# Kernel optimization log

Hardware: AMD Instinct MI355X
Metric: run time of the kernel (lower is better)

## Reference

```python
import jax, jax.numpy as jnp
import numpy as np

B, N, D = 1, 2048, 1024
L, H, DH = 4, 16, 64
INNER = H * DH            # 1024, == D
FF = int(D * 4.0)         # 4096 (GEGLU inner)
SCALE = DH ** -0.5
LN_EPS = 1e-5


def setup_inputs() -> dict:
    key = jax.random.key(0)
    ks = jax.random.split(key, 8)
    w = 0.02
    inp = {
        'x': jax.random.normal(ks[0], (B, N, D), jnp.float32),
        'mask': jnp.ones((B, N), dtype=bool),
        # stacked per-layer params (leading dim L)
        'Wqkv': jax.random.normal(ks[1], (L, D, 3 * INNER), jnp.float32) * w,
        'Wo': jax.random.normal(ks[2], (L, INNER, D), jnp.float32) * w,
        'bo': jnp.zeros((L, D), jnp.float32),
        'ln1_g': jnp.ones((L, D), jnp.float32),
        'ln1_b': jnp.zeros((L, D), jnp.float32),
        'ln2_g': jnp.ones((L, D), jnp.float32),
        'ln2_b': jnp.zeros((L, D), jnp.float32),
        'ls1': jnp.full((L, D), 0.1, jnp.float32),  # LayerScale init_eps=0.1 (depth<=18)
        'ls2': jnp.full((L, D), 0.1, jnp.float32),
        'W1': jax.random.normal(ks[3], (L, D, 2 * FF), jnp.float32) * w,
        'b1': jnp.zeros((L, 2 * FF), jnp.float32),
        'W2': jax.random.normal(ks[4], (L, FF, D), jnp.float32) * w,
        'b2': jnp.zeros((L, D), jnp.float32),
    }
    return inp


def _layernorm(x, g, b):
    mu = jnp.mean(x, axis=-1, keepdims=True)
    var = jnp.mean(jnp.square(x - mu), axis=-1, keepdims=True)
    return (x - mu) * jax.lax.rsqrt(var + LN_EPS) * g + b


def _forward(x, mask, Wqkv, Wo, bo, ln1_g, ln1_b, ln2_g, ln2_b, ls1, ls2, W1, b1, W2, b2):
    n = x.shape[1]
    causal = jnp.arange(n)[None, :] > jnp.arange(n)[:, None]  # True = masked
    valid = mask[:, None, None, :] & ~causal[None, None]       # (B,1,N,N) True = keep
    for l in range(L):
        # --- attention sublayer: x + LayerScale(PreNorm(Attn))(x) ---
        h = _layernorm(x, ln1_g[l], ln1_b[l])
        qkv = h @ Wqkv[l]                                      # (B,N,3*INNER)
        q, k, v = jnp.split(qkv, 3, axis=-1)
        q = q.reshape(B, n, H, DH).transpose(0, 2, 1, 3) * SCALE
        k = k.reshape(B, n, H, DH).transpose(0, 2, 1, 3)
        v = v.reshape(B, n, H, DH).transpose(0, 2, 1, 3)
        dots = jnp.einsum('bhid,bhjd->bhij', q, k)             # (B,H,N,N)
        neg = -jnp.finfo(dots.dtype).max
        dots = jnp.where(valid, dots, neg)
        attn = jax.nn.softmax(dots, axis=-1)                   # stable_softmax, temp=1
        o = jnp.einsum('bhij,bhjd->bhid', attn, v)
        o = o.transpose(0, 2, 1, 3).reshape(B, n, INNER)
        o = o @ Wo[l] + bo[l]
        x = x + o * ls1[l]
        # --- feedforward sublayer: x + LayerScale(PreNorm(GEGLU-FFN))(x) ---
        h = _layernorm(x, ln2_g[l], ln2_b[l])
        u = h @ W1[l] + b1[l]                                  # (B,N,2*FF)
        a, g = jnp.split(u, 2, axis=-1)
        f = (a * jax.nn.gelu(g, approximate=False)) @ W2[l] + b2[l]
        x = x + f * ls2[l]
    return x


def reference(x, mask, Wqkv, Wo, bo, ln1_g, ln1_b, ln2_g, ln2_b, ls1, ls2, W1, b1, W2, b2):
    return _forward(x, mask, Wqkv, Wo, bo, ln1_g, ln1_b, ln2_g, ln2_b, ls1, ls2, W1, b1, W2, b2)
```

## Files before the change

### kernel.cpp

```cpp
#include <hip/hip_runtime.h>
#include <hip/hip_bf16.h>
#include <math.h>

#define LN_EPS 1e-5f
#define ATT_SCALE 0.125f

typedef __bf16 bf16x8 __attribute__((ext_vector_type(8)));
typedef float f32x4 __attribute__((ext_vector_type(4)));

__device__ __forceinline__ unsigned short f2bf(float f){
  unsigned int u = __builtin_bit_cast(unsigned int, f);
  u += 0x7fffu + ((u >> 16) & 1u);
  return (unsigned short)(u >> 16);
}
__device__ __forceinline__ float bfbits2f(unsigned int lo16){
  return __builtin_bit_cast(float, lo16 << 16);
}

__global__ __launch_bounds__(256) void ln_kernel(
    const float* __restrict__ X, const float* __restrict__ g,
    const float* __restrict__ b, unsigned short* __restrict__ H)
{
  __shared__ float red[4];
  int row = blockIdx.x, t = threadIdx.x;
  const float4 xv = ((const float4*)(X + (size_t)row*1024))[t];
  float s = xv.x + xv.y + xv.z + xv.w;
  #pragma unroll
  for (int o=32;o;o>>=1) s += __shfl_down(s,o);
  if ((t&63)==0) red[t>>6] = s;
  __syncthreads();
  float mu = (red[0]+red[1]+red[2]+red[3]) * (1.f/1024.f);
  __syncthreads();
  float dx = xv.x-mu, dy = xv.y-mu, dz = xv.z-mu, dw = xv.w-mu;
  float s2 = dx*dx+dy*dy+dz*dz+dw*dw;
  #pragma unroll
  for (int o=32;o;o>>=1) s2 += __shfl_down(s2,o);
  if ((t&63)==0) red[t>>6] = s2;
  __syncthreads();
  float var = (red[0]+red[1]+red[2]+red[3]) * (1.f/1024.f);
  float rs = rsqrtf(var + LN_EPS);
  const float4 gv = ((const float4*)g)[t];
  const float4 bv = ((const float4*)b)[t];
  ushort4 o4;
  o4.x = f2bf(dx*rs*gv.x + bv.x);
  o4.y = f2bf(dy*rs*gv.y + bv.y);
  o4.z = f2bf(dz*rs*gv.z + bv.z);
  o4.w = f2bf(dw*rs*gv.w + bv.w);
  ((ushort4*)(H + (size_t)row*1024))[t] = o4;
}

template<int SK, int DO_LN>
__global__ __launch_bounds__(256) void redln_kernel(
    const unsigned short* __restrict__ P, float* __restrict__ X,
    const float* __restrict__ bias, const float* __restrict__ scale,
    const float* __restrict__ g, const float* __restrict__ b,
    unsigned short* __restrict__ H)
{
  __shared__ float red[4];
  int row = blockIdx.x, t = threadIdx.x;
  size_t off = (size_t)row*1024 + t*4;
  float4 xv = *(const float4*)(X + off);
  float4 pv;
  {
    uint2 u = *(const uint2*)(P + off);
    pv.x = bfbits2f(u.x & 0xffffu); pv.y = bfbits2f(u.x >> 16);
    pv.z = bfbits2f(u.y & 0xffffu); pv.w = bfbits2f(u.y >> 16);
  }
  #pragma unroll
  for (int c=1;c<SK;c++){
    uint2 u = *(const uint2*)(P + (size_t)c*2048*1024 + off);
    pv.x += bfbits2f(u.x & 0xffffu); pv.y += bfbits2f(u.x >> 16);
    pv.z += bfbits2f(u.y & 0xffffu); pv.w += bfbits2f(u.y >> 16);
  }
  const float4 bv = ((const float4*)bias)[t];
  const float4 sv = ((const float4*)scale)[t];
  xv.x += (pv.x+bv.x)*sv.x;
  xv.y += (pv.y+bv.y)*sv.y;
  xv.z += (pv.z+bv.z)*sv.z;
  xv.w += (pv.w+bv.w)*sv.w;
  *(float4*)(X + off) = xv;
  if (DO_LN){
    float s = xv.x + xv.y + xv.z + xv.w;
    #pragma unroll
    for (int o=32;o;o>>=1) s += __shfl_down(s,o);
    if ((t&63)==0) red[t>>6] = s;
    __syncthreads();
    float mu = (red[0]+red[1]+red[2]+red[3]) * (1.f/1024.f);
    __syncthreads();
    float dx = xv.x-mu, dy = xv.y-mu, dz = xv.z-mu, dw = xv.w-mu;
    float s2 = dx*dx+dy*dy+dz*dz+dw*dw;
    #pragma unroll
    for (int o=32;o;o>>=1) s2 += __shfl_down(s2,o);
    if ((t&63)==0) red[t>>6] = s2;
    __syncthreads();
    float var = (red[0]+red[1]+red[2]+red[3]) * (1.f/1024.f);
    float rs = rsqrtf(var + LN_EPS);
    const float4 gv = ((const float4*)g)[t];
    const float4 lbv = ((const float4*)b)[t];
    ushort4 o4;
    o4.x = f2bf(dx*rs*gv.x + lbv.x);
    o4.y = f2bf(dy*rs*gv.y + lbv.y);
    o4.z = f2bf(dz*rs*gv.z + lbv.z);
    o4.w = f2bf(dw*rs*gv.w + lbv.w);
    ((ushort4*)(H + (size_t)row*1024))[t] = o4;
  }
}

__global__ __launch_bounds__(256) void trc_kernel(
    const float* __restrict__ W, unsigned short* __restrict__ WT, int K, int N)
{
  __shared__ float tile[64][65];
  int n0 = blockIdx.x*64, k0 = blockIdx.y*64;
  int t = threadIdx.x;
  int tx = t & 63, ty = t >> 6;
  #pragma unroll
  for (int p=0;p<16;p++){
    int r = ty*16+p;
    tile[r][tx] = W[(size_t)(k0+r)*N + n0 + tx];
  }
  __syncthreads();
  int kc = t & 31, tb = t >> 5;
  #pragma unroll
  for (int p=0;p<8;p++){
    int nr = tb + p*8;
    unsigned int lo = f2bf(tile[2*kc][nr]);
    unsigned int hi = f2bf(tile[2*kc+1][nr]);
    ((unsigned int*)(WT + (size_t)(n0+nr)*K + k0))[kc] = lo | (hi<<16);
  }
}

__global__ __launch_bounds__(256) void trc_w1_kernel(
    const float* __restrict__ W, unsigned short* __restrict__ WT)
{
  __shared__ float tile[64][65];
  int n0 = blockIdx.x*64, k0 = blockIdx.y*64;
  int ca = (n0>>5)*16;
  int t = threadIdx.x;
  int tx = t & 63, ty = t >> 6;
  #pragma unroll
  for (int p=0;p<16;p++){
    int r = ty*16+p;
    int col = (tx < 32) ? (ca + tx) : (ca + 4064 + tx);
    tile[r][tx] = W[(size_t)(k0+r)*8192 + col];
  }
  __syncthreads();
  int kc = t & 31, tb = t >> 5;
  #pragma unroll
  for (int p=0;p<8;p++){
    int nr = tb + p*8;
    int rr = nr & 31;
    int vcol = (nr>>5)*16 + (rr&15) + ((rr>>4)<<5);
    unsigned int lo = f2bf(tile[2*kc][vcol]);
    unsigned int hi = f2bf(tile[2*kc+1][vcol]);
    ((unsigned int*)(WT + (size_t)(n0+nr)*1024 + k0))[kc] = lo | (hi<<16);
  }
}

template<int MODE, int SWZ>
__global__ __launch_bounds__(256) void gemm_bt(
    const unsigned short* __restrict__ A, const unsigned short* __restrict__ BT,
    int M, int N, int K,
    unsigned short* __restrict__ Obf,
    const float* __restrict__ bias)
{
  __shared__ unsigned short Asm[2][128*64];
  __shared__ unsigned short Bsm[2][128*64];
  int t = threadIdx.x;
  int lane = t & 63;
  int w = t >> 6, wm = w >> 1, wn = w & 1;

  int bn, bm;
  if (SWZ){
    int nwg = gridDim.x * gridDim.y;
    int wg = blockIdx.y * gridDim.x + blockIdx.x;
    int cpx = nwg >> 3;
    int swz = (wg & 7) * cpx + (wg >> 3);
    bn = swz % gridDim.x; bm = swz / gridDim.x;
  } else {
    bn = blockIdx.x; bm = blockIdx.y;
  }

  f32x4 acc[4][4] = {};
  int ktBeg = 0, ktEnd = K >> 6;
  if (MODE == 3){
    int per = (K >> 6) / gridDim.z;
    ktBeg = blockIdx.z * per;
    ktEnd = ktBeg + per;
  }

  int srow = t >> 3, ssc = t & 7;
  auto STAGE = [&](int kt, int buf){
    #pragma unroll
    for (int c=0;c<4;c++){
      int row = c*32 + srow;
      int gc = ssc ^ (row & 7);
      const unsigned short* sa = A  + (size_t)(bm*128 + row)*K + kt*64 + gc*8;
      const unsigned short* sb = BT + (size_t)(bn*128 + row)*K + kt*64 + gc*8;
      __builtin_amdgcn_global_load_lds(
        (const __attribute__((address_space(1))) unsigned int*)sa,
        (__attribute__((address_space(3))) unsigned int*)(&Asm[buf][(c*256 + (t & ~63))*8]),
        16, 0, 0);
      __builtin_amdgcn_global_load_lds(
        (const __attribute__((address_space(1))) unsigned int*)sb,
        (__attribute__((address_space(3))) unsigned int*)(&Bsm[buf][(c*256 + (t & ~63))*8]),
        16, 0, 0);
    }
  };

  STAGE(ktBeg, 0);
  __syncthreads();
  int cur = 0;
  for (int kt = ktBeg; kt < ktEnd; ++kt){
    if (kt + 1 < ktEnd) STAGE(kt + 1, cur ^ 1);
    #pragma unroll
    for (int kk=0;kk<2;kk++){
      bf16x8 aF[4], bF[4];
      #pragma unroll
      for (int m=0;m<4;m++){
        int row = wm*64 + m*16 + (lane&15);
        int ch = kk*4 + (lane>>4);
        aF[m] = *(const bf16x8*)&Asm[cur][row*64 + (ch ^ (row&7))*8];
      }
      #pragma unroll
      for (int n=0;n<4;n++){
        int row = wn*64 + n*16 + (lane&15);
        int ch = kk*4 + (lane>>4);
        bF[n] = *(const bf16x8*)&Bsm[cur][row*64 + (ch ^ (row&7))*8];
      }
      __builtin_amdgcn_s_setprio(1);
      #pragma unroll
      for (int m=0;m<4;m++)
        #pragma unroll
        for (int n=0;n<4;n++)
          acc[m][n] = __builtin_amdgcn_mfma_f32_16x16x32_bf16(aF[m], bF[n], acc[m][n], 0,0,0);
      __builtin_amdgcn_s_setprio(0);
    }
    __syncthreads();
    cur ^= 1;
  }

  int colg = lane & 15;
  if (MODE==4){
    float b1a[2], b1g[2];
    #pragma unroll
    for (int p=0;p<2;p++){
      int oc = (bn*4 + wn*2 + p)*16 + colg;
      b1a[p] = bias[oc];
      b1g[p] = bias[oc + 4096];
    }
    #pragma unroll
    for (int m=0;m<4;m++){
      int gr0 = bm*128 + wm*64 + m*16 + (lane>>4)*4;
      #pragma unroll
      for (int p=0;p<2;p++){
        int ocol = (bn*4 + wn*2 + p)*16 + colg;
        #pragma unroll
        for (int j=0;j<4;j++){
          float va = acc[m][2*p][j]   + b1a[p];
          float vg = acc[m][2*p+1][j] + b1g[p];
          float f = va * (0.5f * vg * (1.f + erff(vg * 0.70710678118f)));
          Obf[(size_t)(gr0+j)*4096 + ocol] = f2bf(f);
        }
      }
    }
    return;
  }
  #pragma unroll
  for (int m=0;m<4;m++){
    int gr0 = bm*128 + wm*64 + m*16 + (lane>>4)*4;
    #pragma unroll
    for (int n=0;n<4;n++){
      int gc = bn*128 + wn*64 + n*16 + colg;
      #pragma unroll
      for (int j=0;j<4;j++){
        int gr = gr0 + j;
        float v = acc[m][n][j];
        if (MODE==0){
          Obf[(size_t)gr*N + gc] = f2bf(v);
        } else {
          Obf[(size_t)blockIdx.z*((size_t)M*N) + (size_t)gr*N + gc] = f2bf(v);
        }
      }
    }
  }
}

__global__ __launch_bounds__(256) void vtr_kernel(
    const unsigned short* __restrict__ qkv, unsigned short* __restrict__ VT)
{
  __shared__ unsigned int tile[64][33];
  int h = blockIdx.y;
  int n0 = blockIdx.x * 64;
  int t = threadIdx.x;
  #pragma unroll
  for (int p=0;p<8;p++){
    int idx = p*256 + t;
    int r = idx >> 5, c = idx & 31;
    tile[r][c] = *(const unsigned int*)(qkv + (size_t)(n0+r)*3072 + 2048 + h*64 + c*2);
  }
  __syncthreads();
  #pragma unroll
  for (int p=0;p<8;p++){
    int idx = p*256 + t;
    int d = idx >> 5, c = idx & 31;
    unsigned int a = tile[2*c][d>>1];
    unsigned int b = tile[2*c+1][d>>1];
    unsigned int lo = (d&1) ? (a>>16) : (a & 0xffffu);
    unsigned int hi = (d&1) ? (b>>16) : (b & 0xffffu);
    *(unsigned int*)(VT + (size_t)h*131072 + (size_t)d*2048 + n0 + c*2) = lo | (hi<<16);
  }
}

__global__ __launch_bounds__(256) void flash_attn(
    const unsigned short* __restrict__ qkv,
    const unsigned short* __restrict__ VT,
    unsigned short* __restrict__ O)
{
  __shared__ unsigned short Klds[2][64*64];
  __shared__ unsigned short Vlds[2][64*64];
  __shared__ unsigned short Plds[4][16*72];
  __shared__ float fbuf[4][16];
  __shared__ float lbuf[4][16];

  int t = threadIdx.x;
  int lane = t & 63;
  int w = t >> 6;
  int q15 = lane & 15, l16 = lane >> 4;

  int bid = blockIdx.x;
  int x = bid & 7, r = bid >> 3;
  int h = 2*x + (r & 1);
  int q = r >> 1;
  int qt = (q < 16) ? q : 47 - q;
  int q0 = qt * 64;

  bf16x8 qF[2];
  int qrow = q0 + w*16 + q15;
  #pragma unroll
  for (int db=0; db<2; db++)
    qF[db] = *(const bf16x8*)(qkv + (size_t)qrow*3072 + h*64 + db*32 + l16*8);

  int srow = t >> 3, ssc = t & 7;
  auto STAGE = [&](int kt, int buf){
    int k0 = kt*64;
    #pragma unroll
    for (int c=0;c<2;c++){
      int row = c*32 + srow;
      int gc = ssc ^ (row & 7);
      const unsigned short* sk = qkv + (size_t)(k0+row)*3072 + 1024 + h*64 + gc*8;
      const unsigned short* sv = VT + (size_t)h*131072 + (size_t)row*2048 + k0 + gc*8;
      __builtin_amdgcn_global_load_lds(
        (const __attribute__((address_space(1))) unsigned int*)sk,
        (__attribute__((address_space(3))) unsigned int*)(&Klds[buf][(c*256 + (t & ~63))*8]),
        16, 0, 0);
      __builtin_amdgcn_global_load_lds(
        (const __attribute__((address_space(1))) unsigned int*)sv,
        (__attribute__((address_space(3))) unsigned int*)(&Vlds[buf][(c*256 + (t & ~63))*8]),
        16, 0, 0);
    }
  };

  f32x4 o[4] = {};
  float m_run = -1e30f, l_run = 0.f;

  STAGE(0, 0);
  __syncthreads();
  int cur = 0;
  for (int kt = 0; kt <= qt; ++kt){
    if (kt < qt) STAGE(kt + 1, cur ^ 1);

    f32x4 s[4] = {};
    #pragma unroll
    for (int km=0;km<4;km++){
      #pragma unroll
      for (int db=0;db<2;db++){
        int row = km*16 + q15;
        int ch = db*4 + l16;
        bf16x8 kF = *(const bf16x8*)&Klds[cur][row*64 + (ch ^ (row&7))*8];
        s[km] = __builtin_amdgcn_mfma_f32_16x16x32_bf16(kF, qF[db], s[km], 0,0,0);
      }
    }

    bool diag = (kt == qt);
    float pmax = -1e30f;
    #pragma unroll
    for (int km=0;km<4;km++){
      #pragma unroll
      for (int j=0;j<4;j++){
        float sv = s[km][j] * ATT_SCALE;
        if (diag){
          int kg = km*16 + l16*4 + j;
          int qg = w*16 + q15;
          if (kg > qg) sv = -1e30f;
        }
        s[km][j] = sv;
        pmax = fmaxf(pmax, sv);
      }
    }
    pmax = fmaxf(pmax, __shfl_xor(pmax, 16));
    pmax = fmaxf(pmax, __shfl_xor(pmax, 32));

    float m_new = fmaxf(m_run, pmax);
    float f = __expf(m_run - m_new);

    float lsum = 0.f;
    #pragma unroll
    for (int km=0;km<4;km++){
      float p0 = __expf(s[km][0]-m_new);
      float p1 = __expf(s[km][1]-m_new);
      float p2 = __expf(s[km][2]-m_new);
      float p3 = __expf(s[km][3]-m_new);
      lsum += (p0+p1)+(p2+p3);
      unsigned int u0 = (unsigned int)f2bf(p0) | ((unsigned int)f2bf(p1)<<16);
      unsigned int u1 = (unsigned int)f2bf(p2) | ((unsigned int)f2bf(p3)<<16);
      *(uint2*)&Plds[w][q15*72 + km*16 + l16*4] = make_uint2(u0,u1);
    }
    lsum += __shfl_xor(lsum,16);
    lsum += __shfl_xor(lsum,32);
    l_run = l_run * f + lsum;
    m_run = m_new;

    if (l16 == 0) fbuf[w][q15] = f;
    f32x4 fv = *(f32x4*)&fbuf[w][l16*4];
    #pragma unroll
    for (int n=0;n<4;n++) o[n] *= fv;

    #pragma unroll
    for (int kb=0;kb<2;kb++){
      bf16x8 aP = *(const bf16x8*)&Plds[w][q15*72 + kb*32 + l16*8];
      #pragma unroll
      for (int n=0;n<4;n++){
        int row = n*16 + q15;
        int ch = kb*4 + l16;
        bf16x8 vF = *(const bf16x8*)&Vlds[cur][row*64 + (ch ^ (row&7))*8];
        o[n] = __builtin_amdgcn_mfma_f32_16x16x32_bf16(aP, vF, o[n], 0,0,0);
      }
    }
    __syncthreads();
    cur ^= 1;
  }

  if (l16 == 0) lbuf[w][q15] = 1.f / l_run;
  f32x4 lv = *(f32x4*)&lbuf[w][l16*4];

  #pragma unroll
  for (int n=0;n<4;n++){
    #pragma unroll
    for (int j=0;j<4;j++){
      int row = q0 + w*16 + l16*4 + j;
      int col = h*64 + n*16 + q15;
      O[(size_t)row*1024 + col] = f2bf(o[n][j]*lv[j]);
    }
  }
}

extern "C" void kernel_launch(void* const* d_in, const int* in_sizes, int n_in,
                              void* d_out, int out_size, void* d_ws, size_t ws_size,
                              hipStream_t stream)
{
  (void)in_sizes; (void)n_in; (void)out_size; (void)ws_size;
  const float* x_in = (const float*)d_in[0];
  const float* Wqkv = (const float*)d_in[2];
  const float* Wo   = (const float*)d_in[3];
  const float* bo   = (const float*)d_in[4];
  const float* ln1g = (const float*)d_in[5];
  const float* ln1b = (const float*)d_in[6];
  const float* ln2g = (const float*)d_in[7];
  const float* ln2b = (const float*)d_in[8];
  const float* ls1  = (const float*)d_in[9];
  const float* ls2  = (const float*)d_in[10];
  const float* W1   = (const float*)d_in[11];
  const float* b1   = (const float*)d_in[12];
  const float* W2   = (const float*)d_in[13];
  const float* b2   = (const float*)d_in[14];
  float* X = (float*)d_out;

  char* ws = (char*)d_ws;
  unsigned short* WT  = (unsigned short*)(ws);
  unsigned short* hb  = (unsigned short*)(ws + (16u<<20));
  unsigned short* qu  = (unsigned short*)(ws + (20u<<20));
  unsigned short* VTg = (unsigned short*)(ws + (36u<<20));
  unsigned short* of  = (unsigned short*)(ws + (52u<<20));
  unsigned short* PTb = (unsigned short*)(ws + (20u<<20));

  hipMemcpyAsync(d_out, (const void*)x_in, (size_t)2048*1024*4,
                 hipMemcpyDeviceToDevice, stream);

  for (int l = 0; l < 4; ++l){
    if (l == 0)
      ln_kernel<<<2048,256,0,stream>>>(X, ln1g, ln1b, hb);
    trc_kernel<<<dim3(3072/64,1024/64),256,0,stream>>>(Wqkv + (size_t)l*1024*3072, WT, 1024, 3072);
    gemm_bt<0,0><<<dim3(3072/128,2048/128),256,0,stream>>>(hb, WT, 2048,3072,1024,
        qu, nullptr);
    vtr_kernel<<<dim3(32,16),256,0,stream>>>(qu, VTg);
    flash_attn<<<512,256,0,stream>>>(qu, VTg, of);
    trc_kernel<<<dim3(1024/64,1024/64),256,0,stream>>>(Wo + (size_t)l*1024*1024, WT, 1024, 1024);
    gemm_bt<3,1><<<dim3(1024/128,2048/128,2),256,0,stream>>>(of, WT, 2048,1024,1024,
        PTb, nullptr);
    redln_kernel<2,1><<<2048,256,0,stream>>>(PTb, X, bo + l*1024, ls1 + l*1024,
        ln2g + l*1024, ln2b + l*1024, hb);
    trc_w1_kernel<<<dim3(8192/64,1024/64),256,0,stream>>>(W1 + (size_t)l*1024*8192, WT);
    gemm_bt<4,0><<<dim3(8192/128,2048/128),256,0,stream>>>(hb, WT, 2048,8192,1024,
        of, b1 + (size_t)l*8192);
    trc_kernel<<<dim3(1024/64,4096/64),256,0,stream>>>(W2 + (size_t)l*4096*1024, WT, 4096, 1024);
    gemm_bt<3,1><<<dim3(1024/128,2048/128,4),256,0,stream>>>(of, WT, 2048,1024,4096,
        PTb, nullptr);
    if (l < 3)
      redln_kernel<4,1><<<2048,256,0,stream>>>(PTb, X, b2 + l*1024, ls2 + l*1024,
          ln1g + (l+1)*1024, ln1b + (l+1)*1024, hb);
    else
      redln_kernel<4,0><<<2048,256,0,stream>>>(PTb, X, b2 + l*1024, ls2 + l*1024,
          nullptr, nullptr, nullptr);
  }
}
```

Baseline: 789.6 us.

## Add 256x256 8-wave pipelined GEMM for FFN W1/W2 projections

Adds a new 512-thread GEMM kernel with 256x256 output tiles that stages tiles straight into LDS with global_load_lds and interleaves half-tile loads with MFMA quarters behind explicit vmcnt waits and barriers. It replaces the 128x128 kernel for the GEGLU W1 GEMM (fused epilogue moved over) and for the W2 split-K GEMM. The W2 split-K factor goes from 4 to 8, so the reduce kernel now sums 8 partials. The aim is more data reuse per block and better load/compute overlap on the largest GEMMs, at the cost of heavier LDS and register use and a larger partial-sum buffer and reduction.

Measured after the change: 802.2 us. No clear change (+1.6%).

```diff
diff --git a/kernel.cpp b/kernel.cpp
--- a/kernel.cpp
+++ b/kernel.cpp
@@ -240,31 +240,6 @@
   }
 
   int colg = lane & 15;
-  if (MODE==4){
-    float b1a[2], b1g[2];
-    #pragma unroll
-    for (int p=0;p<2;p++){
-      int oc = (bn*4 + wn*2 + p)*16 + colg;
-      b1a[p] = bias[oc];
-      b1g[p] = bias[oc + 4096];
-    }
-    #pragma unroll
-    for (int m=0;m<4;m++){
-      int gr0 = bm*128 + wm*64 + m*16 + (lane>>4)*4;
-      #pragma unroll
-      for (int p=0;p<2;p++){
-        int ocol = (bn*4 + wn*2 + p)*16 + colg;
-        #pragma unroll
-        for (int j=0;j<4;j++){
-          float va = acc[m][2*p][j]   + b1a[p];
-          float vg = acc[m][2*p+1][j] + b1g[p];
-          float f = va * (0.5f * vg * (1.f + erff(vg * 0.70710678118f)));
-          Obf[(size_t)(gr0+j)*4096 + ocol] = f2bf(f);
-        }
-      }
-    }
-    return;
-  }
   #pragma unroll
   for (int m=0;m<4;m++){
     int gr0 = bm*128 + wm*64 + m*16 + (lane>>4)*4;
@@ -280,6 +255,166 @@
         } else {
           Obf[(size_t)blockIdx.z*((size_t)M*N) + (size_t)gr*N + gc] = f2bf(v);
         }
+      }
+    }
+  }
+}
+
+#define G8_BARRIER() do { asm volatile("" ::: "memory"); \
+  __builtin_amdgcn_s_barrier(); asm volatile("" ::: "memory"); \
+  __builtin_amdgcn_sched_barrier(0); } while(0)
+#define G8_VW6() asm volatile("s_waitcnt vmcnt(6)" ::: "memory")
+
+template<int MODE>
+__global__ __launch_bounds__(512,2) void gemm8p(
+    const unsigned short* __restrict__ A, const unsigned short* __restrict__ BT,
+    int M, int N, int K,
+    unsigned short* __restrict__ Obf, const float* __restrict__ bias)
+{
+  __shared__ __attribute__((aligned(16))) unsigned short lds[65536];
+  int t = threadIdx.x;
+  int lane = t & 63;
+  int w = t >> 6;
+  int wm = w >> 2, wn = w & 3;
+  int q15 = lane & 15, l16 = lane >> 4;
+
+  int bn = blockIdx.x, bm = blockIdx.y;
+  int rA0 = bm*256, rB0 = bn*256;
+
+  int nkt = K >> 6, ktBeg = 0;
+  if (MODE == 3){
+    int per = nkt / gridDim.z;
+    ktBeg = blockIdx.z * per;
+    nkt = per;
+  }
+
+  int u0 = (w*2+0)*8 + (lane>>3);
+  int u1 = (w*2+1)*8 + (lane>>3);
+  int c0 = (lane&7) ^ (u0&7);
+  int c1 = (lane&7) ^ (u1&7);
+
+  auto STAGE_A = [&](int ktg, int h, int buf){
+    int r0 = (u0&63) | (h<<6) | ((u0>>6)<<7);
+    int r1 = (u1&63) | (h<<6) | ((u1>>6)<<7);
+    const unsigned short* s0 = A + (size_t)(rA0 + r0)*K + ktg*64 + c0*8;
+    const unsigned short* s1 = A + (size_t)(rA0 + r1)*K + ktg*64 + c1*8;
+    __builtin_amdgcn_global_load_lds(
+      (const __attribute__((address_space(1))) unsigned int*)s0,
+      (__attribute__((address_space(3))) unsigned int*)(&lds[buf*32768 + h*8192 + (w*2+0)*512]),
+      16, 0, 0);
+    __builtin_amdgcn_global_load_lds(
+      (const __attribute__((address_space(1))) unsigned int*)s1,
+      (__attribute__((address_space(3))) unsigned int*)(&lds[buf*32768 + h*8192 + (w*2+1)*512]),
+      16, 0, 0);
+  };
+  auto STAGE_B = [&](int ktg, int h, int buf){
+    int r0 = (u0&31) | (h<<5) | ((u0>>5)<<6);
+    int r1 = (u1&31) | (h<<5) | ((u1>>5)<<6);
+    const unsigned short* s0 = BT + (size_t)(rB0 + r0)*K + ktg*64 + c0*8;
+    const unsigned short* s1 = BT + (size_t)(rB0 + r1)*K + ktg*64 + c1*8;
+    __builtin_amdgcn_global_load_lds(
+      (const __attribute__((address_space(1))) unsigned int*)s0,
+      (__attribute__((address_space(3))) unsigned int*)(&lds[buf*32768 + 16384 + h*8192 + (w*2+0)*512]),
+      16, 0, 0);
+    __builtin_amdgcn_global_load_lds(
+      (const __attribute__((address_space(1))) unsigned int*)s1,
+      (__attribute__((address_space(3))) unsigned int*)(&lds[buf*32768 + 16384 + h*8192 + (w*2+1)*512]),
+      16, 0, 0);
+  };
+
+  f32x4 acc[8][4] = {};
+  bf16x8 aF[4][2], bF0[2][2], bF1[2][2];
+
+#define G8_LOAD_AF(H, BASE) \
+  _Pragma("unroll") for (int m=0;m<4;m++){ \
+    int u = m*16 + q15 + wm*64; \
+    _Pragma("unroll") for (int kk=0;kk<2;kk++) \
+      aF[m][kk] = *(const bf16x8*)&lds[(BASE) + (H)*8192 + u*64 + (((kk*4+l16) ^ (u&7))*8)]; }
+#define G8_LOAD_BF(DST, H, BASE) \
+  _Pragma("unroll") for (int nn=0;nn<2;nn++){ \
+    int u = nn*16 + q15 + wn*32; \
+    _Pragma("unroll") for (int kk=0;kk<2;kk++) \
+      DST[nn][kk] = *(const bf16x8*)&lds[(BASE) + 16384 + (H)*8192 + u*64 + (((kk*4+l16) ^ (u&7))*8)]; }
+#define G8_QMFMA(MB, NB, BF) \
+  __builtin_amdgcn_s_setprio(1); \
+  _Pragma("unroll") for (int m=0;m<4;m++) \
+  _Pragma("unroll") for (int nn=0;nn<2;nn++) \
+  _Pragma("unroll") for (int kk=0;kk<2;kk++) \
+    acc[(MB)+m][(NB)+nn] = __builtin_amdgcn_mfma_f32_16x16x32_bf16( \
+        aF[m][kk], BF[nn][kk], acc[(MB)+m][(NB)+nn], 0,0,0); \
+  __builtin_amdgcn_s_setprio(0);
+
+  STAGE_A(ktBeg+0, 0, 0);
+  STAGE_A(ktBeg+0, 1, 0);
+  STAGE_B(ktBeg+0, 0, 0);
+  STAGE_B(ktBeg+0, 1, 0);
+  if (nkt > 1) STAGE_B(ktBeg+1, 0, 1);
+  asm volatile("s_waitcnt vmcnt(2)" ::: "memory");
+  G8_BARRIER();
+
+  for (int kt = 0; kt < nkt; ++kt){
+    int buf = kt & 1, obuf = buf ^ 1;
+    int base = buf * 32768;
+    if (kt + 1 < nkt) STAGE_A(ktBeg+kt+1, 0, obuf);
+    G8_VW6();
+    G8_BARRIER();
+    G8_LOAD_AF(0, base);
+    G8_LOAD_BF(bF0, 0, base);
+    G8_QMFMA(0, 0, bF0);
+    G8_BARRIER();
+    if (kt + 1 < nkt) STAGE_A(ktBeg+kt+1, 1, obuf);
+    G8_VW6();
+    G8_BARRIER();
+    G8_LOAD_BF(bF1, 1, base);
+    G8_QMFMA(0, 2, bF1);
+    G8_BARRIER();
+    if (kt + 1 < nkt) STAGE_B(ktBeg+kt+1, 1, obuf);
+    G8_VW6();
+    G8_BARRIER();
+    G8_LOAD_AF(1, base);
+    G8_QMFMA(4, 0, bF0);
+    G8_BARRIER();
+    if (kt + 2 < nkt) STAGE_B(ktBeg+kt+2, 0, buf);
+    G8_VW6();
+    G8_BARRIER();
+    G8_QMFMA(4, 2, bF1);
+    G8_BARRIER();
+  }
+
+  if (MODE == 4){
+    float b1a[2], b1g[2];
+    #pragma unroll
+    for (int p=0;p<2;p++){
+      int oc = (bn*8 + wn*2 + p)*16 + q15;
+      b1a[p] = bias[oc];
+      b1g[p] = bias[oc + 4096];
+    }
+    #pragma unroll
+    for (int m=0;m<8;m++){
+      int gr0 = bm*256 + wm*128 + m*16 + l16*4;
+      #pragma unroll
+      for (int p=0;p<2;p++){
+        int ocol = (bn*8 + wn*2 + p)*16 + q15;
+        #pragma unroll
+        for (int j=0;j<4;j++){
+          float va = acc[m][2*p][j]   + b1a[p];
+          float vg = acc[m][2*p+1][j] + b1g[p];
+          float f = va * (0.5f * vg * (1.f + erff(vg * 0.70710678118f)));
+          Obf[(size_t)(gr0+j)*4096 + ocol] = f2bf(f);
+        }
+      }
+    }
+  } else {
+    size_t zoff = (size_t)blockIdx.z * ((size_t)M*N);
+    #pragma unroll
+    for (int m=0;m<8;m++){
+      int gr0 = bm*256 + wm*128 + m*16 + l16*4;
+      #pragma unroll
+      for (int n=0;n<4;n++){
+        int gc = bn*256 + wn*64 + n*16 + q15;
+        #pragma unroll
+        for (int j=0;j<4;j++)
+          Obf[zoff + (size_t)(gr0+j)*N + gc] = f2bf(acc[m][n][j]);
       }
     }
   }
@@ -411,9 +546,9 @@
       float p2 = __expf(s[km][2]-m_new);
       float p3 = __expf(s[km][3]-m_new);
       lsum += (p0+p1)+(p2+p3);
-      unsigned int u0 = (unsigned int)f2bf(p0) | ((unsigned int)f2bf(p1)<<16);
-      unsigned int u1 = (unsigned int)f2bf(p2) | ((unsigned int)f2bf(p3)<<16);
-      *(uint2*)&Plds[w][q15*72 + km*16 + l16*4] = make_uint2(u0,u1);
+      unsigned int v0 = (unsigned int)f2bf(p0) | ((unsigned int)f2bf(p1)<<16);
+      unsigned int v1 = (unsigned int)f2bf(p2) | ((unsigned int)f2bf(p3)<<16);
+      *(uint2*)&Plds[w][q15*72 + km*16 + l16*4] = make_uint2(v0,v1);
     }
     lsum += __shfl_xor(lsum,16);
     lsum += __shfl_xor(lsum,32);
@@ -500,16 +635,16 @@
     redln_kernel<2,1><<<2048,256,0,stream>>>(PTb, X, bo + l*1024, ls1 + l*1024,
         ln2g + l*1024, ln2b + l*1024, hb);
     trc_w1_kernel<<<dim3(8192/64,1024/64),256,0,stream>>>(W1 + (size_t)l*1024*8192, WT);
-    gemm_bt<4,0><<<dim3(8192/128,2048/128),256,0,stream>>>(hb, WT, 2048,8192,1024,
+    gemm8p<4><<<dim3(8192/256,2048/256),512,0,stream>>>(hb, WT, 2048,8192,1024,
         of, b1 + (size_t)l*8192);
     trc_kernel<<<dim3(1024/64,4096/64),256,0,stream>>>(W2 + (size_t)l*4096*1024, WT, 4096, 1024);
-    gemm_bt<3,1><<<dim3(1024/128,2048/128,4),256,0,stream>>>(of, WT, 2048,1024,4096,
+    gemm8p<3><<<dim3(1024/256,2048/256,8),512,0,stream>>>(of, WT, 2048,1024,4096,
         PTb, nullptr);
     if (l < 3)
-      redln_kernel<4,1><<<2048,256,0,stream>>>(PTb, X, b2 + l*1024, ls2 + l*1024,
+      redln_kernel<8,1><<<2048,256,0,stream>>>(PTb, X, b2 + l*1024, ls2 + l*1024,
           ln1g + (l+1)*1024, ln1b + (l+1)*1024, hb);
     else
-      redln_kernel<4,0><<<2048,256,0,stream>>>(PTb, X, b2 + l*1024, ls2 + l*1024,
+      redln_kernel<8,0><<<2048,256,0,stream>>>(PTb, X, b2 + l*1024, ls2 + l*1024,
           nullptr, nullptr, nullptr);
   }
 }
```

## Add 256x256 8-wave GEMM with direct-to-LDS loads for FFN, batch weight transposes

Applied to the files above, without the earlier changes.

Adds a new 512-thread GEMM kernel with 256x256 tiles that loads global memory straight into LDS with a swizzled layout and a phased barrier schedule. The FFN up-projection (with fused GEGLU) and down-projection now use it, and the down-projection split-K grows to 8 slices, so the reduce/LN kernel now sums 8 partials. All per-layer weight transposes/bf16 conversions are hoisted into four batched launches before the layer loop, each with its own workspace buffer. This aims to cut launch count and raise GEMM data reuse, at the cost of a larger workspace and more split-K partial traffic.

Result: no change. 803.3 us (+1.7%).

```diff
diff --git a/kernel.cpp b/kernel.cpp
--- a/kernel.cpp
+++ b/kernel.cpp
@@ -110,13 +110,15 @@
     const float* __restrict__ W, unsigned short* __restrict__ WT, int K, int N)
 {
   __shared__ float tile[64][65];
+  const float* Wz = W + (size_t)blockIdx.z*K*N;
+  unsigned short* WTz = WT + (size_t)blockIdx.z*K*N;
   int n0 = blockIdx.x*64, k0 = blockIdx.y*64;
   int t = threadIdx.x;
   int tx = t & 63, ty = t >> 6;
   #pragma unroll
   for (int p=0;p<16;p++){
     int r = ty*16+p;
-    tile[r][tx] = W[(size_t)(k0+r)*N + n0 + tx];
+    tile[r][tx] = Wz[(size_t)(k0+r)*N + n0 + tx];
   }
   __syncthreads();
   int kc = t & 31, tb = t >> 5;
@@ -125,7 +127,7 @@
     int nr = tb + p*8;
     unsigned int lo = f2bf(tile[2*kc][nr]);
     unsigned int hi = f2bf(tile[2*kc+1][nr]);
-    ((unsigned int*)(WT + (size_t)(n0+nr)*K + k0))[kc] = lo | (hi<<16);
+    ((unsigned int*)(WTz + (size_t)(n0+nr)*K + k0))[kc] = lo | (hi<<16);
   }
 }
 
@@ -133,6 +135,8 @@
     const float* __restrict__ W, unsigned short* __restrict__ WT)
 {
   __shared__ float tile[64][65];
+  const float* Wz = W + (size_t)blockIdx.z*1024*8192;
+  unsigned short* WTz = WT + (size_t)blockIdx.z*1024*8192;
   int n0 = blockIdx.x*64, k0 = blockIdx.y*64;
   int ca = (n0>>5)*16;
   int t = threadIdx.x;
@@ -141,7 +145,7 @@
   for (int p=0;p<16;p++){
     int r = ty*16+p;
     int col = (tx < 32) ? (ca + tx) : (ca + 4064 + tx);
-    tile[r][tx] = W[(size_t)(k0+r)*8192 + col];
+    tile[r][tx] = Wz[(size_t)(k0+r)*8192 + col];
   }
   __syncthreads();
   int kc = t & 31, tb = t >> 5;
@@ -152,7 +156,7 @@
     int vcol = (nr>>5)*16 + (rr&15) + ((rr>>4)<<5);
     unsigned int lo = f2bf(tile[2*kc][vcol]);
     unsigned int hi = f2bf(tile[2*kc+1][vcol]);
-    ((unsigned int*)(WT + (size_t)(n0+nr)*1024 + k0))[kc] = lo | (hi<<16);
+    ((unsigned int*)(WTz + (size_t)(n0+nr)*1024 + k0))[kc] = lo | (hi<<16);
   }
 }
 
@@ -240,31 +244,6 @@
   }
 
   int colg = lane & 15;
-  if (MODE==4){
-    float b1a[2], b1g[2];
-    #pragma unroll
-    for (int p=0;p<2;p++){
-      int oc = (bn*4 + wn*2 + p)*16 + colg;
-      b1a[p] = bias[oc];
-      b1g[p] = bias[oc + 4096];
-    }
-    #pragma unroll
-    for (int m=0;m<4;m++){
-      int gr0 = bm*128 + wm*64 + m*16 + (lane>>4)*4;
-      #pragma unroll
-      for (int p=0;p<2;p++){
-        int ocol = (bn*4 + wn*2 + p)*16 + colg;
-        #pragma unroll
-        for (int j=0;j<4;j++){
-          float va = acc[m][2*p][j]   + b1a[p];
-          float vg = acc[m][2*p+1][j] + b1g[p];
-          float f = va * (0.5f * vg * (1.f + erff(vg * 0.70710678118f)));
-          Obf[(size_t)(gr0+j)*4096 + ocol] = f2bf(f);
-        }
-      }
-    }
-    return;
-  }
   #pragma unroll
   for (int m=0;m<4;m++){
     int gr0 = bm*128 + wm*64 + m*16 + (lane>>4)*4;
@@ -280,6 +259,151 @@
         } else {
           Obf[(size_t)blockIdx.z*((size_t)M*N) + (size_t)gr*N + gc] = f2bf(v);
         }
+      }
+    }
+  }
+}
+
+#define FENCE() asm volatile("" ::: "memory")
+#define VW4() asm volatile("s_waitcnt vmcnt(4)" ::: "memory")
+#define VW0() asm volatile("s_waitcnt vmcnt(0)" ::: "memory")
+
+template<int MODE>
+__global__ __launch_bounds__(512,2) void gemm8p(
+    const unsigned short* __restrict__ A, const unsigned short* __restrict__ BT,
+    int M, int N, int K,
+    unsigned short* __restrict__ Obf, const float* __restrict__ bias)
+{
+  __shared__ __attribute__((aligned(16))) unsigned short lds[65536];
+  int t = threadIdx.x;
+  int lane = t & 63;
+  int w = t >> 6;
+  int wm = w >> 2, wn = w & 3;
+  int q15 = lane & 15, l16 = lane >> 4;
+
+  int bn = blockIdx.x, bm = blockIdx.y;
+  int rA0 = bm*256, rB0 = bn*256;
+
+  int nkt = K >> 6, ktBeg = 0;
+  if (MODE == 3){
+    int per = nkt / gridDim.z;
+    ktBeg = blockIdx.z * per;
+    nkt = per;
+  }
+
+  auto STG = [&](const unsigned short* Mat, int r0, int ktg, int kk, int slot, int isB){
+    int base = (isB?32768:0) + slot*16384 + kk*8192;
+    #pragma unroll
+    for (int i=0;i<2;i++){
+      int lam = i*512 + t;
+      int row = lam >> 2, c = lam & 3;
+      int g = c ^ (row&3) ^ ((row>>2)&3);
+      const unsigned short* src = Mat + (size_t)(r0+row)*K + (ktBeg+ktg)*64 + kk*32 + g*8;
+      __builtin_amdgcn_global_load_lds(
+        (const __attribute__((address_space(1))) unsigned int*)src,
+        (__attribute__((address_space(3))) unsigned int*)(&lds[base + (i*512 + (t & ~63))*8]),
+        16, 0, 0);
+    }
+  };
+
+  f32x4 acc[8][4] = {};
+  bf16x8 aF[4], bF[4];
+
+  auto RD_A = [&](int mh, int kk, int slot){
+    #pragma unroll
+    for (int m=0;m<4;m++){
+      int r = wm*128 + (mh*4+m)*16 + q15;
+      int c = l16 ^ (r&3) ^ ((r>>2)&3);
+      aF[m] = *(const bf16x8*)&lds[slot*16384 + kk*8192 + r*32 + c*8];
+    }
+  };
+  auto RD_B = [&](int kk, int slot){
+    #pragma unroll
+    for (int n=0;n<4;n++){
+      int r = wn*64 + n*16 + q15;
+      int c = l16 ^ (r&3) ^ ((r>>2)&3);
+      bF[n] = *(const bf16x8*)&lds[32768 + slot*16384 + kk*8192 + r*32 + c*8];
+    }
+  };
+  auto MF = [&](int mb){
+    __builtin_amdgcn_s_setprio(1);
+    #pragma unroll
+    for (int m=0;m<4;m++)
+      #pragma unroll
+      for (int n=0;n<4;n++)
+        acc[mb+m][n] = __builtin_amdgcn_mfma_f32_16x16x32_bf16(aF[m], bF[n], acc[mb+m][n], 0,0,0);
+    __builtin_amdgcn_s_setprio(0);
+  };
+  auto BAR = [&](){ FENCE(); __builtin_amdgcn_s_barrier(); FENCE(); };
+
+  STG(A, rA0, 0, 0, 0, 0);
+  STG(BT, rB0, 0, 0, 0, 1);
+  STG(A, rA0, 0, 1, 0, 0);
+  STG(BT, rB0, 0, 1, 0, 1);
+  VW4();
+  BAR();
+
+  for (int kt = 0; kt < nkt; ++kt){
+    int s = kt & 1, os = s ^ 1;
+    bool st = (kt + 1 < nkt);
+    if (st) STG(A, rA0, kt+1, 0, os, 0);
+    RD_A(0, 0, s); RD_B(0, s);
+    BAR();
+    MF(0);
+    BAR();
+    if (st) STG(BT, rB0, kt+1, 0, os, 1);
+    RD_A(1, 0, s);
+    BAR();
+    MF(4);
+    if (st) { VW4(); } else { VW0(); }
+    BAR();
+    if (st) STG(A, rA0, kt+1, 1, os, 0);
+    RD_A(0, 1, s); RD_B(1, s);
+    BAR();
+    MF(0);
+    BAR();
+    if (st) STG(BT, rB0, kt+1, 1, os, 1);
+    RD_A(1, 1, s);
+    BAR();
+    MF(4);
+    if (st) VW4();
+    BAR();
+  }
+
+  if (MODE == 4){
+    float b1a[2], b1g[2];
+    #pragma unroll
+    for (int p=0;p<2;p++){
+      int oc = (bn*8 + wn*2 + p)*16 + q15;
+      b1a[p] = bias[oc];
+      b1g[p] = bias[oc + 4096];
+    }
+    #pragma unroll
+    for (int m=0;m<8;m++){
+      int gr0 = bm*256 + wm*128 + m*16 + l16*4;
+      #pragma unroll
+      for (int p=0;p<2;p++){
+        int ocol = (bn*8 + wn*2 + p)*16 + q15;
+        #pragma unroll
+        for (int j=0;j<4;j++){
+          float va = acc[m][2*p][j]   + b1a[p];
+          float vg = acc[m][2*p+1][j] + b1g[p];
+          float f = va * (0.5f * vg * (1.f + erff(vg * 0.70710678118f)));
+          Obf[(size_t)(gr0+j)*4096 + ocol] = f2bf(f);
+        }
+      }
+    }
+  } else {
+    size_t zoff = (size_t)blockIdx.z * ((size_t)M*N);
+    #pragma unroll
+    for (int m=0;m<8;m++){
+      int gr0 = bm*256 + wm*128 + m*16 + l16*4;
+      #pragma unroll
+      for (int n=0;n<4;n++){
+        int gc = bn*256 + wn*64 + n*16 + q15;
+        #pragma unroll
+        for (int j=0;j<4;j++)
+          Obf[zoff + (size_t)(gr0+j)*N + gc] = f2bf(acc[m][n][j]);
       }
     }
   }
@@ -411,9 +535,9 @@
       float p2 = __expf(s[km][2]-m_new);
       float p3 = __expf(s[km][3]-m_new);
       lsum += (p0+p1)+(p2+p3);
-      unsigned int u0 = (unsigned int)f2bf(p0) | ((unsigned int)f2bf(p1)<<16);
-      unsigned int u1 = (unsigned int)f2bf(p2) | ((unsigned int)f2bf(p3)<<16);
-      *(uint2*)&Plds[w][q15*72 + km*16 + l16*4] = make_uint2(u0,u1);
+      unsigned int v0 = (unsigned int)f2bf(p0) | ((unsigned int)f2bf(p1)<<16);
+      unsigned int v1 = (unsigned int)f2bf(p2) | ((unsigned int)f2bf(p3)<<16);
+      *(uint2*)&Plds[w][q15*72 + km*16 + l16*4] = make_uint2(v0,v1);
     }
     lsum += __shfl_xor(lsum,16);
     lsum += __shfl_xor(lsum,32);
@@ -476,40 +600,44 @@
   float* X = (float*)d_out;
 
   char* ws = (char*)d_ws;
-  unsigned short* WT  = (unsigned short*)(ws);
-  unsigned short* hb  = (unsigned short*)(ws + (16u<<20));
-  unsigned short* qu  = (unsigned short*)(ws + (20u<<20));
-  unsigned short* VTg = (unsigned short*)(ws + (36u<<20));
-  unsigned short* of  = (unsigned short*)(ws + (52u<<20));
-  unsigned short* PTb = (unsigned short*)(ws + (20u<<20));
+  unsigned short* WTq = (unsigned short*)(ws);
+  unsigned short* WTo = (unsigned short*)(ws + (24u<<20));
+  unsigned short* WT1 = (unsigned short*)(ws + (32u<<20));
+  unsigned short* WT2 = (unsigned short*)(ws + (96u<<20));
+  unsigned short* hb  = (unsigned short*)(ws + (128u<<20));
+  unsigned short* qu  = (unsigned short*)(ws + (132u<<20));
+  unsigned short* VTg = (unsigned short*)(ws + (144u<<20));
+  unsigned short* of  = (unsigned short*)(ws + (148u<<20));
+  unsigned short* PTb = (unsigned short*)(ws + (164u<<20));
 
   hipMemcpyAsync(d_out, (const void*)x_in, (size_t)2048*1024*4,
                  hipMemcpyDeviceToDevice, stream);
+
+  trc_kernel<<<dim3(3072/64,1024/64,4),256,0,stream>>>(Wqkv, WTq, 1024, 3072);
+  trc_kernel<<<dim3(1024/64,1024/64,4),256,0,stream>>>(Wo,   WTo, 1024, 1024);
+  trc_w1_kernel<<<dim3(8192/64,1024/64,4),256,0,stream>>>(W1, WT1);
+  trc_kernel<<<dim3(1024/64,4096/64,4),256,0,stream>>>(W2,   WT2, 4096, 1024);
 
   for (int l = 0; l < 4; ++l){
     if (l == 0)
       ln_kernel<<<2048,256,0,stream>>>(X, ln1g, ln1b, hb);
-    trc_kernel<<<dim3(3072/64,1024/64),256,0,stream>>>(Wqkv + (size_t)l*1024*3072, WT, 1024, 3072);
-    gemm_bt<0,0><<<dim3(3072/128,2048/128),256,0,stream>>>(hb, WT, 2048,3072,1024,
-        qu, nullptr);
+    gemm_bt<0,0><<<dim3(3072/128,2048/128),256,0,stream>>>(hb, WTq + (size_t)l*3072*1024,
+        2048,3072,1024, qu, nullptr);
     vtr_kernel<<<dim3(32,16),256,0,stream>>>(qu, VTg);
     flash_attn<<<512,256,0,stream>>>(qu, VTg, of);
-    trc_kernel<<<dim3(1024/64,1024/64),256,0,stream>>>(Wo + (size_t)l*1024*1024, WT, 1024, 1024);
-    gemm_bt<3,1><<<dim3(1024/128,2048/128,2),256,0,stream>>>(of, WT, 2048,1024,1024,
-        PTb, nullptr);
+    gemm_bt<3,1><<<dim3(1024/128,2048/128,2),256,0,stream>>>(of, WTo + (size_t)l*1024*1024,
+        2048,1024,1024, PTb, nullptr);
     redln_kernel<2,1><<<2048,256,0,stream>>>(PTb, X, bo + l*1024, ls1 + l*1024,
         ln2g + l*1024, ln2b + l*1024, hb);
-    trc_w1_kernel<<<dim3(8192/64,1024/64),256,0,stream>>>(W1 + (size_t)l*1024*8192, WT);
-    gemm_bt<4,0><<<dim3(8192/128,2048/128),256,0,stream>>>(hb, WT, 2048,8192,1024,
-        of, b1 + (size_t)l*8192);
-    trc_kernel<<<dim3(1024/64,4096/64),256,0,stream>>>(W2 + (size_t)l*4096*1024, WT, 4096, 1024);
-    gemm_bt<3,1><<<dim3(1024/128,2048/128,4),256,0,stream>>>(of, WT, 2048,1024,4096,
-        PTb, nullptr);
+    gemm8p<4><<<dim3(8192/256,2048/256),512,0,stream>>>(hb, WT1 + (size_t)l*8192*1024,
+        2048,8192,1024, of, b1 + (size_t)l*8192);
+    gemm8p<3><<<dim3(1024/256,2048/256,8),512,0,stream>>>(of, WT2 + (size_t)l*1024*4096,
+        2048,1024,4096, PTb, nullptr);
     if (l < 3)
-      redln_kernel<4,1><<<2048,256,0,stream>>>(PTb, X, b2 + l*1024, ls2 + l*1024,
+      redln_kernel<8,1><<<2048,256,0,stream>>>(PTb, X, b2 + l*1024, ls2 + l*1024,
           ln1g + (l+1)*1024, ln1b + (l+1)*1024, hb);
     else
-      redln_kernel<4,0><<<2048,256,0,stream>>>(PTb, X, b2 + l*1024, ls2 + l*1024,
+      redln_kernel<8,0><<<2048,256,0,stream>>>(PTb, X, b2 + l*1024, ls2 + l*1024,
           nullptr, nullptr, nullptr);
   }
 }
```

## Batch weight transposes upfront and stage GEMM epilogue through LDS for coalesced stores

Applied to the files above, without the earlier changes.

All four layers' weight transpose/bf16 conversions now run as four batched launches before the layer loop, each writing into its own workspace region, instead of sixteen per-layer launches into a shared buffer. This cuts launch count and gives the transposes larger grids. The GEMM epilogue now writes bf16 results into shared memory first and then emits 16-byte coalesced global stores, replacing scattered 2-byte stores. The cost is a much larger workspace footprint and an extra barrier plus LDS round trip in every GEMM.

After: 796.6 us. About the same (+0.9%).

```diff
diff --git a/kernel.cpp b/kernel.cpp
--- a/kernel.cpp
+++ b/kernel.cpp
@@ -110,13 +110,15 @@
     const float* __restrict__ W, unsigned short* __restrict__ WT, int K, int N)
 {
   __shared__ float tile[64][65];
+  const float* Wz = W + (size_t)blockIdx.z*K*N;
+  unsigned short* WTz = WT + (size_t)blockIdx.z*K*N;
   int n0 = blockIdx.x*64, k0 = blockIdx.y*64;
   int t = threadIdx.x;
   int tx = t & 63, ty = t >> 6;
   #pragma unroll
   for (int p=0;p<16;p++){
     int r = ty*16+p;
-    tile[r][tx] = W[(size_t)(k0+r)*N + n0 + tx];
+    tile[r][tx] = Wz[(size_t)(k0+r)*N + n0 + tx];
   }
   __syncthreads();
   int kc = t & 31, tb = t >> 5;
@@ -125,7 +127,7 @@
     int nr = tb + p*8;
     unsigned int lo = f2bf(tile[2*kc][nr]);
     unsigned int hi = f2bf(tile[2*kc+1][nr]);
-    ((unsigned int*)(WT + (size_t)(n0+nr)*K + k0))[kc] = lo | (hi<<16);
+    ((unsigned int*)(WTz + (size_t)(n0+nr)*K + k0))[kc] = lo | (hi<<16);
   }
 }
 
@@ -133,6 +135,8 @@
     const float* __restrict__ W, unsigned short* __restrict__ WT)
 {
   __shared__ float tile[64][65];
+  const float* Wz = W + (size_t)blockIdx.z*1024*8192;
+  unsigned short* WTz = WT + (size_t)blockIdx.z*1024*8192;
   int n0 = blockIdx.x*64, k0 = blockIdx.y*64;
   int ca = (n0>>5)*16;
   int t = threadIdx.x;
@@ -141,7 +145,7 @@
   for (int p=0;p<16;p++){
     int r = ty*16+p;
     int col = (tx < 32) ? (ca + tx) : (ca + 4064 + tx);
-    tile[r][tx] = W[(size_t)(k0+r)*8192 + col];
+    tile[r][tx] = Wz[(size_t)(k0+r)*8192 + col];
   }
   __syncthreads();
   int kc = t & 31, tb = t >> 5;
@@ -152,7 +156,7 @@
     int vcol = (nr>>5)*16 + (rr&15) + ((rr>>4)<<5);
     unsigned int lo = f2bf(tile[2*kc][vcol]);
     unsigned int hi = f2bf(tile[2*kc+1][vcol]);
-    ((unsigned int*)(WT + (size_t)(n0+nr)*1024 + k0))[kc] = lo | (hi<<16);
+    ((unsigned int*)(WTz + (size_t)(n0+nr)*1024 + k0))[kc] = lo | (hi<<16);
   }
 }
 
@@ -239,7 +243,9 @@
     cur ^= 1;
   }
 
+  unsigned short* ep = &Asm[0][0];
   int colg = lane & 15;
+  int r0 = wm*64 + (lane>>4)*4;
   if (MODE==4){
     float b1a[2], b1g[2];
     #pragma unroll
@@ -250,38 +256,43 @@
     }
     #pragma unroll
     for (int m=0;m<4;m++){
-      int gr0 = bm*128 + wm*64 + m*16 + (lane>>4)*4;
       #pragma unroll
       for (int p=0;p<2;p++){
-        int ocol = (bn*4 + wn*2 + p)*16 + colg;
+        int cw = (wn*2 + p)*16 + colg;
         #pragma unroll
         for (int j=0;j<4;j++){
           float va = acc[m][2*p][j]   + b1a[p];
           float vg = acc[m][2*p+1][j] + b1g[p];
           float f = va * (0.5f * vg * (1.f + erff(vg * 0.70710678118f)));
-          Obf[(size_t)(gr0+j)*4096 + ocol] = f2bf(f);
+          ep[(r0 + m*16 + j)*64 + cw] = f2bf(f);
         }
       }
     }
+    __syncthreads();
+    #pragma unroll
+    for (int i=0;i<4;i++){
+      int idx = i*256 + t;
+      int row = idx >> 3, ch = idx & 7;
+      *(uint4*)&Obf[(size_t)(bm*128+row)*4096 + bn*64 + ch*8] = *(const uint4*)&ep[row*64 + ch*8];
+    }
     return;
   }
   #pragma unroll
-  for (int m=0;m<4;m++){
-    int gr0 = bm*128 + wm*64 + m*16 + (lane>>4)*4;
+  for (int m=0;m<4;m++)
     #pragma unroll
     for (int n=0;n<4;n++){
-      int gc = bn*128 + wn*64 + n*16 + colg;
-      #pragma unroll
-      for (int j=0;j<4;j++){
-        int gr = gr0 + j;
-        float v = acc[m][n][j];
-        if (MODE==0){
-          Obf[(size_t)gr*N + gc] = f2bf(v);
-        } else {
-          Obf[(size_t)blockIdx.z*((size_t)M*N) + (size_t)gr*N + gc] = f2bf(v);
-        }
-      }
-    }
+      int cw = wn*64 + n*16 + colg;
+      #pragma unroll
+      for (int j=0;j<4;j++)
+        ep[(r0 + m*16 + j)*128 + cw] = f2bf(acc[m][n][j]);
+    }
+  __syncthreads();
+  size_t zoff = (MODE==3) ? (size_t)blockIdx.z*((size_t)M*N) : 0;
+  #pragma unroll
+  for (int i=0;i<8;i++){
+    int idx = i*256 + t;
+    int row = idx >> 4, ch = idx & 15;
+    *(uint4*)&Obf[zoff + (size_t)(bm*128+row)*N + bn*128 + ch*8] = *(const uint4*)&ep[row*128 + ch*8];
   }
 }
 
@@ -411,9 +422,9 @@
       float p2 = __expf(s[km][2]-m_new);
       float p3 = __expf(s[km][3]-m_new);
       lsum += (p0+p1)+(p2+p3);
-      unsigned int u0 = (unsigned int)f2bf(p0) | ((unsigned int)f2bf(p1)<<16);
-      unsigned int u1 = (unsigned int)f2bf(p2) | ((unsigned int)f2bf(p3)<<16);
-      *(uint2*)&Plds[w][q15*72 + km*16 + l16*4] = make_uint2(u0,u1);
+      unsigned int v0 = (unsigned int)f2bf(p0) | ((unsigned int)f2bf(p1)<<16);
+      unsigned int v1 = (unsigned int)f2bf(p2) | ((unsigned int)f2bf(p3)<<16);
+      *(uint2*)&Plds[w][q15*72 + km*16 + l16*4] = make_uint2(v0,v1);
     }
     lsum += __shfl_xor(lsum,16);
     lsum += __shfl_xor(lsum,32);
@@ -476,35 +487,39 @@
   float* X = (float*)d_out;
 
   char* ws = (char*)d_ws;
-  unsigned short* WT  = (unsigned short*)(ws);
-  unsigned short* hb  = (unsigned short*)(ws + (16u<<20));
-  unsigned short* qu  = (unsigned short*)(ws + (20u<<20));
-  unsigned short* VTg = (unsigned short*)(ws + (36u<<20));
-  unsigned short* of  = (unsigned short*)(ws + (52u<<20));
-  unsigned short* PTb = (unsigned short*)(ws + (20u<<20));
+  unsigned short* WTq = (unsigned short*)(ws);
+  unsigned short* WTo = (unsigned short*)(ws + (24u<<20));
+  unsigned short* WT1 = (unsigned short*)(ws + (32u<<20));
+  unsigned short* WT2 = (unsigned short*)(ws + (96u<<20));
+  unsigned short* hb  = (unsigned short*)(ws + (128u<<20));
+  unsigned short* qu  = (unsigned short*)(ws + (132u<<20));
+  unsigned short* VTg = (unsigned short*)(ws + (144u<<20));
+  unsigned short* of  = (unsigned short*)(ws + (148u<<20));
+  unsigned short* PTb = (unsigned short*)(ws + (164u<<20));
 
   hipMemcpyAsync(d_out, (const void*)x_in, (size_t)2048*1024*4,
                  hipMemcpyDeviceToDevice, stream);
+
+  trc_kernel<<<dim3(3072/64,1024/64,4),256,0,stream>>>(Wqkv, WTq, 1024, 3072);
+  trc_kernel<<<dim3(1024/64,1024/64,4),256,0,stream>>>(Wo,   WTo, 1024, 1024);
+  trc_w1_kernel<<<dim3(8192/64,1024/64,4),256,0,stream>>>(W1, WT1);
+  trc_kernel<<<dim3(1024/64,4096/64,4),256,0,stream>>>(W2,   WT2, 4096, 1024);
 
   for (int l = 0; l < 4; ++l){
     if (l == 0)
       ln_kernel<<<2048,256,0,stream>>>(X, ln1g, ln1b, hb);
-    trc_kernel<<<dim3(3072/64,1024/64),256,0,stream>>>(Wqkv + (size_t)l*1024*3072, WT, 1024, 3072);
-    gemm_bt<0,0><<<dim3(3072/128,2048/128),256,0,stream>>>(hb, WT, 2048,3072,1024,
-        qu, nullptr);
+    gemm_bt<0,0><<<dim3(3072/128,2048/128),256,0,stream>>>(hb, WTq + (size_t)l*3072*1024,
+        2048,3072,1024, qu, nullptr);
     vtr_kernel<<<dim3(32,16),256,0,stream>>>(qu, VTg);
     flash_attn<<<512,256,0,stream>>>(qu, VTg, of);
-    trc_kernel<<<dim3(1024/64,1024/64),256,0,stream>>>(Wo + (size_t)l*1024*1024, WT, 1024, 1024);
-    gemm_bt<3,1><<<dim3(1024/128,2048/128,2),256,0,stream>>>(of, WT, 2048,1024,1024,
-        PTb, nullptr);
+    gemm_bt<3,1><<<dim3(1024/128,2048/128,2),256,0,stream>>>(of, WTo + (size_t)l*1024*1024,
+        2048,1024,1024, PTb, nullptr);
     redln_kernel<2,1><<<2048,256,0,stream>>>(PTb, X, bo + l*1024, ls1 + l*1024,
         ln2g + l*1024, ln2b + l*1024, hb);
-    trc_w1_kernel<<<dim3(8192/64,1024/64),256,0,stream>>>(W1 + (size_t)l*1024*8192, WT);
-    gemm_bt<4,0><<<dim3(8192/128,2048/128),256,0,stream>>>(hb, WT, 2048,8192,1024,
-        of, b1 + (size_t)l*8192);
-    trc_kernel<<<dim3(1024/64,4096/64),256,0,stream>>>(W2 + (size_t)l*4096*1024, WT, 4096, 1024);
-    gemm_bt<3,1><<<dim3(1024/128,2048/128,4),256,0,stream>>>(of, WT, 2048,1024,4096,
-        PTb, nullptr);
+    gemm_bt<4,0><<<dim3(8192/128,2048/128),256,0,stream>>>(hb, WT1 + (size_t)l*8192*1024,
+        2048,8192,1024, of, b1 + (size_t)l*8192);
+    gemm_bt<3,1><<<dim3(1024/128,2048/128,4),256,0,stream>>>(of, WT2 + (size_t)l*1024*4096,
+        2048,1024,4096, PTb, nullptr);
     if (l < 3)
       redln_kernel<4,1><<<2048,256,0,stream>>>(PTb, X, b2 + l*1024, ls2 + l*1024,
           ln1g + (l+1)*1024, ln1b + (l+1)*1024, hb);
```
